# Kernel optimization log

Measured on AMD Instinct MI355X. Metric: run time of the kernel, lower is better.

## Reference

```python
import jax, jax.numpy as jnp
import numpy as np


def _build_tree(N: int, n: int, seed: int = 0):
    """Random forest encoded as parent pointers + sibling ranks.

    parents:  int32 [N+1]; parents[i] in [0, i) for i>0, root(0) and sentinel(N) -> N.
    child_pos: int32 [N+1]; rank among siblings (in_edges order); >= n means the
               one-hot code is all zeros (matches torch.eye rows beyond n, and roots).
    """
    rng = np.random.default_rng(seed)
    parents = np.empty(N + 1, dtype=np.int32)
    parents[0] = N                      # root -> sentinel
    parents[1:N] = rng.integers(0, np.arange(1, N))  # parent of i is an earlier node
    parents[N] = N                      # sentinel self-loop

    pa = parents[:N].astype(np.int64)
    order = np.argsort(pa, kind="stable")
    sorted_pa = pa[order]
    _, first_idx, inv = np.unique(sorted_pa, return_index=True, return_inverse=True)
    rank = np.arange(N) - first_idx[inv]           # sibling rank within each parent group
    child_pos = np.empty(N + 1, dtype=np.int32)
    child_pos[order] = rank.astype(np.int32)
    child_pos[0] = n                    # root has no parent -> zero code
    child_pos[N] = n                    # sentinel -> zero code
    return parents, child_pos


def setup_inputs() -> dict:
    N, n, k = 262144, 32, 16
    parents, child_pos = _build_tree(N, n)
    return {
        "parents": jnp.asarray(parents),
        "child_pos": jnp.asarray(child_pos),
        "n": n,
        "k": k,
    }


def reference(parents, child_pos, n, k):
    """pos_embeds[node] = concat_{t=0..k-1} onehot(child_pos(ancestor_t(node)), n).

    This is the closed form of the original layer-by-layer scatter:
      pos[child, :n]  = eye row (sibling rank one-hot)
      pos[child, n:]  = pos[parent, :-n]
    Roots keep all-zero codes (child_pos = n -> out-of-range one-hot = zeros).
    """
    N = parents.shape[0] - 1

    def step(cur, _):
        code = jax.nn.one_hot(child_pos[cur], n, dtype=jnp.float32)  # [N, n]
        return parents[cur], code

    _, codes = jax.lax.scan(step, jnp.arange(N, dtype=parents.dtype), None, length=k)
    # codes: [k, N, n] -> [N, k*n] with slot 0 (own code) first
    return jnp.transpose(codes, (1, 0, 2)).reshape(N, k * n)
```

## Files before the change

### kernel.cpp

```cpp
#include <hip/hip_runtime.h>


#define NN 32
#define KK 16
#define NPB 256

__global__ __launch_bounds__(256, 8) void pe_kernel(
    const int* __restrict__ parents,
    const int* __restrict__ child_pos,
    float* __restrict__ out, int N)
{
    __shared__ unsigned char codes[NPB * KK];

    const int tid   = threadIdx.x;
    const int node0 = blockIdx.x * NPB;
    const int node  = node0 + tid;

    unsigned int packed[KK / 4];
    if (node < N) {
        int cur = node;
        #pragma unroll
        for (int w = 0; w < KK / 4; ++w) {
            unsigned int u = 0;
            #pragma unroll
            for (int b = 0; b < 4; ++b) {
                int cp = child_pos[cur];
                unsigned int byte = (cp < NN) ? (unsigned int)cp : 0xFFu;
                u |= byte << (8 * b);
                cur = parents[cur];
            }
            packed[w] = u;
        }
    } else {
        #pragma unroll
        for (int w = 0; w < KK / 4; ++w) packed[w] = 0xFFFFFFFFu;
    }
    *reinterpret_cast<uint4*>(&codes[tid * KK]) =
        make_uint4(packed[0], packed[1], packed[2], packed[3]);
    __syncthreads();

    const int t_seg = (tid >> 3) & 15;
    const int q4    = (tid & 7) * 4;
    const int hi    = tid >> 7;
    float4* out4 = reinterpret_cast<float4*>(out) + (size_t)node0 * (NN * KK / 4);

    #pragma unroll 4
    for (int iter = 0; iter < (NPB * KK * NN / 4) / 256; ++iter) {
        const int nl   = 2 * iter + hi;
        const int code = codes[nl * KK + t_seg];
        float4 v;
        v.x = (code == q4    ) ? 1.0f : 0.0f;
        v.y = (code == q4 + 1) ? 1.0f : 0.0f;
        v.z = (code == q4 + 2) ? 1.0f : 0.0f;
        v.w = (code == q4 + 3) ? 1.0f : 0.0f;
        if (node0 + nl < N)
            out4[(size_t)iter * 256 + tid] = v;
    }
}

extern "C" void kernel_launch(void* const* d_in, const int* in_sizes, int n_in,
                              void* d_out, int out_size, void* d_ws, size_t ws_size,
                              hipStream_t stream) {
    const int* parents   = (const int*)d_in[0];
    const int* child_pos = (const int*)d_in[1];
    float* out = (float*)d_out;

    const int N    = in_sizes[0] - 1;
    const int grid = (N + NPB - 1) / NPB;

    pe_kernel<<<grid, 256, 0, stream>>>(parents, child_pos, out, N);
}
```

Before: 114.0 us.

## Split codes gather and one-hot expansion into separate kernels with nontemporal stores

Splits the fused kernel in two. The first kernel walks the ancestor chain and writes packed byte codes to workspace. The second is a grid-stride expansion kernel that streams the one-hot float4 output with nontemporal stores. The goal is to separate the latency-bound pointer chasing from the bandwidth-bound output write so that each phase can use the whole GPU. The cost is an extra kernel launch plus a 4MB workspace round trip, and the fused path is kept as a fallback when the workspace is too small.

```diff
diff --git a/kernel.cpp b/kernel.cpp
--- a/kernel.cpp
+++ b/kernel.cpp
@@ -5,13 +5,57 @@
 #define KK 16
 #define NPB 256
 
+typedef float f32x4 __attribute__((ext_vector_type(4)));
+
+__global__ __launch_bounds__(256) void pe_codes(
+    const int* __restrict__ parents,
+    const int* __restrict__ child_pos,
+    uint4* __restrict__ codes_out, int N)
+{
+    const int node = blockIdx.x * blockDim.x + threadIdx.x;
+    if (node >= N) return;
+    unsigned int packed[KK / 4];
+    int cur = node;
+    #pragma unroll
+    for (int w = 0; w < KK / 4; ++w) {
+        unsigned int u = 0;
+        #pragma unroll
+        for (int b = 0; b < 4; ++b) {
+            int cp = child_pos[cur];
+            unsigned int byte = (cp < NN) ? (unsigned int)cp : 0xFFu;
+            u |= byte << (8 * b);
+            cur = parents[cur];
+        }
+        packed[w] = u;
+    }
+    codes_out[node] = make_uint4(packed[0], packed[1], packed[2], packed[3]);
+}
+
+__global__ __launch_bounds__(256) void pe_expand(
+    const unsigned char* __restrict__ codes,
+    f32x4* __restrict__ out4, size_t total_f4)
+{
+    const size_t stride = (size_t)gridDim.x * blockDim.x;
+    const size_t gid    = (size_t)blockIdx.x * blockDim.x + threadIdx.x;
+    const int q4 = (int)(gid & 7) * 4;
+    #pragma unroll 8
+    for (size_t idx = gid; idx < total_f4; idx += stride) {
+        const int code = codes[idx >> 3];
+        f32x4 v;
+        v.x = (code == q4    ) ? 1.0f : 0.0f;
+        v.y = (code == q4 + 1) ? 1.0f : 0.0f;
+        v.z = (code == q4 + 2) ? 1.0f : 0.0f;
+        v.w = (code == q4 + 3) ? 1.0f : 0.0f;
+        __builtin_nontemporal_store(v, &out4[idx]);
+    }
+}
+
 __global__ __launch_bounds__(256, 8) void pe_kernel(
     const int* __restrict__ parents,
     const int* __restrict__ child_pos,
     float* __restrict__ out, int N)
 {
     __shared__ unsigned char codes[NPB * KK];
-
     const int tid   = threadIdx.x;
     const int node0 = blockIdx.x * NPB;
     const int node  = node0 + tid;
@@ -65,8 +109,17 @@
     const int* child_pos = (const int*)d_in[1];
     float* out = (float*)d_out;
 
-    const int N    = in_sizes[0] - 1;
-    const int grid = (N + NPB - 1) / NPB;
+    const int N = in_sizes[0] - 1;
 
-    pe_kernel<<<grid, 256, 0, stream>>>(parents, child_pos, out, N);
+    if (ws_size >= (size_t)N * KK) {
+        const int grid1 = (N + 255) / 256;
+        pe_codes<<<grid1, 256, 0, stream>>>(parents, child_pos, (uint4*)d_ws, N);
+
+        const size_t total_f4 = (size_t)N * (NN * KK / 4);
+        pe_expand<<<2048, 256, 0, stream>>>(
+            (const unsigned char*)d_ws, (f32x4*)out, total_f4);
+    } else {
+        const int grid = (N + NPB - 1) / NPB;
+        pe_kernel<<<grid, 256, 0, stream>>>(parents, child_pos, out, N);
+    }
 }
```

Measured after the change: 114.6 us. About the same (+0.5%).

## Replace shared-memory code staging with wavefront readlane broadcast

Applied to the files above, without the earlier changes.

Drops the LDS buffer and block barrier. Each wave now broadcasts each node's packed ancestor codes to all lanes with readlane, and every lane writes two float4 one-hot segments per node. This removes shared-memory traffic and __syncthreads, at the cost of 256 scalar readlanes per wave and a different write ordering. The bounds check on stores is gone, so correctness relies on N being a multiple of 64.

```diff
diff --git a/kernel.cpp b/kernel.cpp
--- a/kernel.cpp
+++ b/kernel.cpp
@@ -3,58 +3,64 @@
 
 #define NN 32
 #define KK 16
-#define NPB 256
 
-__global__ __launch_bounds__(256, 8) void pe_kernel(
+typedef float f32x4 __attribute__((ext_vector_type(4)));
+
+__global__ __launch_bounds__(256) void pe_fused_rl(
     const int* __restrict__ parents,
     const int* __restrict__ child_pos,
-    float* __restrict__ out, int N)
+    f32x4* __restrict__ out4, int N)
 {
-    __shared__ unsigned char codes[NPB * KK];
+    const int lane  = (int)(threadIdx.x & 63);
+    const int wid   = (int)((blockIdx.x * blockDim.x + threadIdx.x) >> 6);
+    const int wbase = wid * 64;
+    const int node  = wbase + lane;
 
-    const int tid   = threadIdx.x;
-    const int node0 = blockIdx.x * NPB;
-    const int node  = node0 + tid;
-
-    unsigned int packed[KK / 4];
-    if (node < N) {
-        int cur = node;
+    unsigned int c[4];
+    {
+        int cur = (node < N) ? node : N;
         #pragma unroll
-        for (int w = 0; w < KK / 4; ++w) {
+        for (int w = 0; w < 4; ++w) {
             unsigned int u = 0;
             #pragma unroll
             for (int b = 0; b < 4; ++b) {
-                int cp = child_pos[cur];
-                unsigned int byte = (cp < NN) ? (unsigned int)cp : 0xFFu;
+                const int cp = child_pos[cur];
+                const unsigned int byte = (cp < NN) ? (unsigned int)cp : 0xFFu;
                 u |= byte << (8 * b);
                 cur = parents[cur];
             }
-            packed[w] = u;
+            c[w] = u;
         }
-    } else {
-        #pragma unroll
-        for (int w = 0; w < KK / 4; ++w) packed[w] = 0xFFFFFFFFu;
     }
-    *reinterpret_cast<uint4*>(&codes[tid * KK]) =
-        make_uint4(packed[0], packed[1], packed[2], packed[3]);
-    __syncthreads();
 
-    const int t_seg = (tid >> 3) & 15;
-    const int q4    = (tid & 7) * 4;
-    const int hi    = tid >> 7;
-    float4* out4 = reinterpret_cast<float4*>(out) + (size_t)node0 * (NN * KK / 4);
+    const bool hi32 = (lane >= 32);
+    const int  sh   = ((lane >> 3) & 3) * 8;
+    const int  q4   = (lane & 7) * 4;
+
+    f32x4* wout = out4 + (size_t)wbase * 128 + lane;
 
     #pragma unroll 4
-    for (int iter = 0; iter < (NPB * KK * NN / 4) / 256; ++iter) {
-        const int nl   = 2 * iter + hi;
-        const int code = codes[nl * KK + t_seg];
-        float4 v;
-        v.x = (code == q4    ) ? 1.0f : 0.0f;
-        v.y = (code == q4 + 1) ? 1.0f : 0.0f;
-        v.z = (code == q4 + 2) ? 1.0f : 0.0f;
-        v.w = (code == q4 + 3) ? 1.0f : 0.0f;
-        if (node0 + nl < N)
-            out4[(size_t)iter * 256 + tid] = v;
+    for (int r = 0; r < 64; ++r) {
+        const unsigned s0 = (unsigned)__builtin_amdgcn_readlane((int)c[0], r);
+        const unsigned s1 = (unsigned)__builtin_amdgcn_readlane((int)c[1], r);
+        const unsigned s2 = (unsigned)__builtin_amdgcn_readlane((int)c[2], r);
+        const unsigned s3 = (unsigned)__builtin_amdgcn_readlane((int)c[3], r);
+
+        const int code0 = (int)(((hi32 ? s1 : s0) >> sh) & 0xFFu);
+        const int code1 = (int)(((hi32 ? s3 : s2) >> sh) & 0xFFu);
+
+        f32x4 v0, v1;
+        v0.x = (code0 == q4    ) ? 1.0f : 0.0f;
+        v0.y = (code0 == q4 + 1) ? 1.0f : 0.0f;
+        v0.z = (code0 == q4 + 2) ? 1.0f : 0.0f;
+        v0.w = (code0 == q4 + 3) ? 1.0f : 0.0f;
+        v1.x = (code1 == q4    ) ? 1.0f : 0.0f;
+        v1.y = (code1 == q4 + 1) ? 1.0f : 0.0f;
+        v1.z = (code1 == q4 + 2) ? 1.0f : 0.0f;
+        v1.w = (code1 == q4 + 3) ? 1.0f : 0.0f;
+
+        wout[(size_t)r * 128]      = v0;
+        wout[(size_t)r * 128 + 64] = v1;
     }
 }
 
@@ -63,10 +69,11 @@
                               hipStream_t stream) {
     const int* parents   = (const int*)d_in[0];
     const int* child_pos = (const int*)d_in[1];
-    float* out = (float*)d_out;
+    f32x4* out4 = (f32x4*)d_out;
 
-    const int N    = in_sizes[0] - 1;
-    const int grid = (N + NPB - 1) / NPB;
+    const int N = in_sizes[0] - 1;
+    const int n_waves = (N + 63) / 64;
+    const int grid    = (n_waves + 3) / 4;
 
-    pe_kernel<<<grid, 256, 0, stream>>>(parents, child_pos, out, N);
+    pe_fused_rl<<<grid, 256, 0, stream>>>(parents, child_pos, out4, N);
 }
```

New measurement: 111.3 us. 1.02x faster.
